# Performance work log

Measured on AMD Instinct MI355X. Metric: run time of the kernel, lower is better.

The kernel has to match this reference:

```python
import jax, jax.numpy as jnp
from jax import lax
import numpy as np

B, H, W = 8, 512, 512
COUT = 256          # backbone.out_channels
NPTS = 5 + 6        # num_vertebra_points + num_disc_points
CASC = 3            # num_cascades
PIX_MEAN, PIX_STD = 0.5, 1.0


def setup_inputs() -> dict:
    key = jax.random.key(0)
    k0, k1, k2, k3 = jax.random.split(key, 4)
    images = jax.random.normal(k0, (B, 1, H, W), jnp.float32)
    # stand-in for BackboneWithFPN level '0': stride-4 7x7 conv, 3 -> 256 ch
    backbone_w = jax.random.normal(k1, (COUT, 3, 7, 7), jnp.float32) * 0.05
    backbone_b = jnp.zeros((COUT,), jnp.float32)
    # self.fc: 1x1 conv, 256 -> 11 keypoint score channels
    fc_w = jax.random.normal(k2, (NPTS, COUT), jnp.float32) * 0.05
    fc_b = jnp.zeros((NPTS,), jnp.float32)
    # cascade heads: Linear(256, 2) per cascade
    head_w = jax.random.normal(k3, (CASC, COUT, 2), jnp.float32) * 0.02
    head_b = jnp.zeros((CASC, 2), jnp.float32)
    return dict(images=images, backbone_w=backbone_w, backbone_b=backbone_b,
                fc_w=fc_w, fc_b=fc_b, head_w=head_w, head_b=head_b)


def _resize_bilinear_ac(x, oh, ow):
    # bilinear, align_corners=True, matching F.interpolate
    b, c, h, w = x.shape
    ys = jnp.linspace(0.0, h - 1.0, oh)
    xs = jnp.linspace(0.0, w - 1.0, ow)
    y0 = jnp.floor(ys).astype(jnp.int32); y1 = jnp.minimum(y0 + 1, h - 1)
    x0 = jnp.floor(xs).astype(jnp.int32); x1 = jnp.minimum(x0 + 1, w - 1)
    wy = (ys - y0.astype(x.dtype))[:, None]          # (oh,1)
    wx = (xs - x0.astype(x.dtype))                   # (ow,)
    top = x[:, :, y0, :] * (1.0 - wy) + x[:, :, y1, :] * wy   # (b,c,oh,w)
    return top[:, :, :, x0] * (1.0 - wx) + top[:, :, :, x1] * wx


def _extract_point_feature(fm, coords, height, width):
    # fm: (B,C,fh,fw); coords: (B,P,2) with (width, height) order
    fh, fw = fm.shape[-2:]
    hi = jnp.clip(jnp.round(coords[:, :, 1] * (fh / height)).astype(jnp.int32), 0, fh - 1)
    wi = jnp.clip(jnp.round(coords[:, :, 0] * (fw / width)).astype(jnp.int32), 0, fw - 1)
    fm_t = fm.transpose(0, 2, 3, 1)                  # (B,fh,fw,C)
    return jax.vmap(lambda f, a, b: f[a, b])(fm_t, hi, wi)  # (B,P,C)


def reference(images, backbone_w, backbone_b, fc_w, fc_b, head_w, head_b):
    b = images.shape[0]
    x = (images - PIX_MEAN) / PIX_STD
    x = jnp.broadcast_to(x, (b, 3, H, W))            # .expand(-1,3,-1,-1)
    fm = lax.conv_general_dilated(
        x, backbone_w, window_strides=(4, 4), padding=((3, 3), (3, 3)),
        dimension_numbers=('NCHW', 'OIHW', 'NCHW')) + backbone_b[None, :, None, None]
    scores = jnp.einsum('bchw,kc->bkhw', fm, fc_w) + fc_b[None, :, None, None]
    scores = _resize_bilinear_ac(scores, H, W)
    heat = jax.nn.sigmoid(scores)
    # SpinalModelBase: per-channel argmax -> (width, height) coords
    idx = jnp.argmax(heat.reshape(b, NPTS, -1), axis=-1)
    coords = jnp.stack([idx % W, idx // W], axis=-1).astype(jnp.float32)  # (B,P,2)
    # cascades: gather point features, tiny Linear shift, update coords
    for i in range(CASC):
        feats = _extract_point_feature(fm, coords, H, W)     # (B,P,C)
        shift = feats @ head_w[i] + head_b[i]                # (B,P,2)
        coords = coords + shift
    return coords  # final cascade output, float (B, NPTS, 2)
```

## Files before the change

### kernel.cpp

```cpp
#include <hip/hip_runtime.h>
#include <hip/hip_bf16.h>
#include <math.h>

#define BATCH 8
#define HH 512
#define WW 512
#define COUT 256
#define NPTS 11
#define CASC 3
#define FH 128
#define FW 128
#define KT 49
#define NBK (BATCH*NPTS)
#define NSPLIT 8
#define OROWS (HH/NSPLIT)

#define FOLD_OFF   0
#define SCORES_OFF 1024
#define PVAL_OFF   (1024 + 1441792)
#define PIDX_OFF   (PVAL_OFF + 704)

#define STEPC (127.0f/511.0f)

__global__ __launch_bounds__(256) void fold_kernel(
    const float* __restrict__ bw, const float* __restrict__ bb,
    const float* __restrict__ fcw, const float* __restrict__ fcb,
    const float* __restrict__ hw, const float* __restrict__ hb,
    float* __restrict__ fold) {
  int id = blockIdx.x*4 + (threadIdx.x >> 6);
  if (id >= 850) return;
  int row = id / 50, t = id % 50;
  int lane = threadIdx.x & 63;
  float acc = 0.f;
  for (int c = lane; c < COUT; c += 64) {
    float coef;
    if (row < NPTS) {
      coef = fcw[row*COUT + c];
    } else {
      int r = row - NPTS;
      coef = hw[(r >> 1)*(COUT*2) + c*2 + (r & 1)];
    }
    float wsum;
    if (t < KT) {
      const float* p = bw + c*(3*KT) + t;
      wsum = p[0] + p[KT] + p[2*KT];
    } else {
      wsum = bb[c];
    }
    acc += coef * wsum;
  }
  #pragma unroll
  for (int off = 32; off > 0; off >>= 1) acc += __shfl_down(acc, off);
  if (lane == 0) {
    if (t == KT) acc += (row < NPTS) ? fcb[row] : hb[row - NPTS];
    if (row < NPTS) {
      if (t < KT) fold[row*KT + t] = acc;
      else        fold[NPTS*KT + row] = acc;
    } else {
      int r = row - NPTS;
      if (t < KT) fold[550 + r*KT + t] = acc;
      else        fold[844 + r] = acc;
    }
  }
}

__global__ __launch_bounds__(256) void scores_kernel(
    const float* __restrict__ img, const float* __restrict__ fold,
    float* __restrict__ scores) {
  int g = blockIdx.x*256 + threadIdx.x;
  int b = g >> 14;
  int rem = g & 16383;
  int y = rem >> 7, x = rem & 127;
  const float* im = img + (size_t)b * (HH*WW);
  float acc[NPTS];
  #pragma unroll
  for (int k = 0; k < NPTS; ++k) acc[k] = fold[NPTS*KT + k];
  int iy0 = y*4 - 3, ix0 = x*4 - 3;
  #pragma unroll
  for (int kh = 0; kh < 7; ++kh) {
    int iy = iy0 + kh;
    if (iy < 0 || iy >= HH) continue;
    #pragma unroll
    for (int kw = 0; kw < 7; ++kw) {
      int ix = ix0 + kw;
      if (ix < 0 || ix >= WW) continue;
      float xv = im[iy*WW + ix] - 0.5f;
      int t = kh*7 + kw;
      #pragma unroll
      for (int k = 0; k < NPTS; ++k) acc[k] = fmaf(fold[k*KT + t], xv, acc[k]);
    }
  }
  float* out = scores + (size_t)b * (NPTS*FH*FW) + rem;
  #pragma unroll
  for (int k = 0; k < NPTS; ++k) out[(size_t)k*(FH*FW)] = acc[k];
}

__global__ __launch_bounds__(256) void argmax_kernel(
    const float* __restrict__ scores, float* __restrict__ pval,
    int* __restrict__ pidx) {
  __shared__ __align__(16) float s[20*128];
  __shared__ float wv[4];
  __shared__ int   wi[4];
  int bk = blockIdx.x / NSPLIT;
  int q  = blockIdx.x % NSPLIT;
  const float* src = scores + (size_t)bk * (FH*FW);

  int oyb = q*OROWS;
  int ybase = (int)((float)oyb * STEPC);
  int ylast = (int)((float)(oyb + OROWS - 1) * STEPC);
  int yend  = min(ylast + 1, FH - 1);
  int rows  = yend - ybase + 1;
  {
    const float4* src4 = (const float4*)(src + ybase*FW);
    float4* s4 = (float4*)s;
    int n4 = (rows*FW) >> 2;
    for (int i = threadIdx.x; i < n4; i += 256) s4[i] = src4[i];
  }
  __syncthreads();

  int ox0 = threadIdx.x*2, ox1 = ox0 + 1;
  float tx0 = (float)ox0 * STEPC, tx1 = (float)ox1 * STEPC;
  int xa0 = (int)tx0, xb0 = (int)tx1;
  float wx0 = tx0 - (float)xa0, wx1 = tx1 - (float)xb0;
  int xa1 = min(xa0 + 1, FW - 1), xb1 = min(xb0 + 1, FW - 1);
  float omwx0 = 1.f - wx0, omwx1 = 1.f - wx1;

  float best = -3.4028235e38f;
  int bidx = 0x7fffffff;
  int prevY0 = -1;
  float a0=0.f, b0=0.f, c0=0.f, d0=0.f;
  float a1=0.f, b1=0.f, c1=0.f, d1=0.f;
  for (int j = 0; j < OROWS; ++j) {
    int oy = oyb + j;
    float ty = (float)oy * STEPC;
    int y0 = (int)ty;
    float wy = ty - (float)y0;
    float omwy = 1.f - wy;
    if (y0 != prevY0) {
      int y1 = min(y0 + 1, FH - 1);
      const float* r0 = s + (y0 - ybase)*FW;
      const float* r1 = s + (y1 - ybase)*FW;
      a0 = r0[xa0]; b0 = r1[xa0]; c0 = r0[xa1]; d0 = r1[xa1];
      a1 = r0[xb0]; b1 = r1[xb0]; c1 = r0[xb1]; d1 = r1[xb1];
      prevY0 = y0;
    }
    {
      float top0 = a0*omwy + b0*wy;
      float top1 = c0*omwy + d0*wy;
      float v = top0*omwx0 + top1*wx0;
      if (v > best) { best = v; bidx = oy*512 + ox0; }
    }
    {
      float top0 = a1*omwy + b1*wy;
      float top1 = c1*omwy + d1*wy;
      float v = top0*omwx1 + top1*wx1;
      if (v > best) { best = v; bidx = oy*512 + ox1; }
    }
  }

  #pragma unroll
  for (int off = 32; off > 0; off >>= 1) {
    float ov = __shfl_down(best, off);
    int   oi = __shfl_down(bidx, off);
    if (ov > best || (ov == best && oi < bidx)) { best = ov; bidx = oi; }
  }
  int wave = threadIdx.x >> 6;
  if ((threadIdx.x & 63) == 0) { wv[wave] = best; wi[wave] = bidx; }
  __syncthreads();
  if (threadIdx.x == 0) {
    best = wv[0]; bidx = wi[0];
    #pragma unroll
    for (int w = 1; w < 4; ++w) {
      float ov = wv[w]; int oi = wi[w];
      if (ov > best || (ov == best && oi < bidx)) { best = ov; bidx = oi; }
    }
    pval[bk*NSPLIT + q] = best;
    pidx[bk*NSPLIT + q] = bidx;
  }
}

__global__ __launch_bounds__(128) void cascade_kernel(
    const float* __restrict__ img, const float* __restrict__ fold,
    const float* __restrict__ pval, const int* __restrict__ pidx,
    float* __restrict__ out) {
  int p = threadIdx.x;
  if (p >= NBK) return;
  float best = pval[p*NSPLIT]; int bidx = pidx[p*NSPLIT];
  #pragma unroll
  for (int q = 1; q < NSPLIT; ++q) {
    float v = pval[p*NSPLIT + q]; int i = pidx[p*NSPLIT + q];
    if (v > best || (v == best && i < bidx)) { best = v; bidx = i; }
  }
  float cx = (float)(bidx & 511);
  float cy = (float)(bidx >> 9);
  int b = p / NPTS;
  const float* im = img + (size_t)b * (HH*WW);
  for (int i = 0; i < CASC; ++i) {
    float ry = rintf(cy * 0.25f), rx = rintf(cx * 0.25f);
    int hi = (int)fminf(fmaxf(ry, 0.f), (float)(FH - 1));
    int wi = (int)fminf(fmaxf(rx, 0.f), (float)(FW - 1));
    float s0 = fold[844 + i*2 + 0];
    float s1 = fold[844 + i*2 + 1];
    int iy0 = hi*4 - 3, ix0 = wi*4 - 3;
    for (int kh = 0; kh < 7; ++kh) {
      int iy = iy0 + kh;
      if (iy < 0 || iy >= HH) continue;
      for (int kw = 0; kw < 7; ++kw) {
        int ix = ix0 + kw;
        if (ix < 0 || ix >= WW) continue;
        float xv = im[iy*WW + ix] - 0.5f;
        int t = kh*7 + kw;
        s0 = fmaf(fold[550 + (i*2 + 0)*KT + t], xv, s0);
        s1 = fmaf(fold[550 + (i*2 + 1)*KT + t], xv, s1);
      }
    }
    cx += s0;
    cy += s1;
  }
  out[p*2 + 0] = cx;
  out[p*2 + 1] = cy;
}

extern "C" void kernel_launch(void* const* d_in, const int* in_sizes, int n_in,
                              void* d_out, int out_size, void* d_ws, size_t ws_size,
                              hipStream_t stream) {
  const float* img = (const float*)d_in[0];
  const float* bw  = (const float*)d_in[1];
  const float* bb  = (const float*)d_in[2];
  const float* fcw = (const float*)d_in[3];
  const float* fcb = (const float*)d_in[4];
  const float* hw  = (const float*)d_in[5];
  const float* hb  = (const float*)d_in[6];
  float* out = (float*)d_out;

  float* ws     = (float*)d_ws;
  float* fold   = ws + FOLD_OFF;
  float* scores = ws + SCORES_OFF;
  float* pval   = ws + PVAL_OFF;
  int*   pidx   = (int*)(ws + PIDX_OFF);

  fold_kernel<<<213, 256, 0, stream>>>(bw, bb, fcw, fcb, hw, hb, fold);
  scores_kernel<<<512, 256, 0, stream>>>(img, fold, scores);
  argmax_kernel<<<NBK*NSPLIT, 256, 0, stream>>>(scores, pval, pidx);
  cascade_kernel<<<1, 128, 0, stream>>>(img, fold, pval, pidx, out);
}
```

Before: 121.8 us.

## Evaluate bilinear argmax only at source-cell endpoint rows and columns

Bilinear interpolation is linear between neighbouring source samples. So the maximum over output pixels within each source cell must sit at the first or last output row and column mapped to that cell. The argmax kernel now has each thread own one endpoint column and loops over source rows, evaluating only the endpoint output rows instead of all upsampled rows and columns. The folded weights are also transposed to a tap-major layout so the per-tap coefficient reads in the scores kernel are contiguous across keypoints. The risk is tie-breaking and rounding differences against a full scan, though results should match in the exact case.

```diff
diff --git a/kernel.cpp b/kernel.cpp
--- a/kernel.cpp
+++ b/kernel.cpp
@@ -54,7 +54,7 @@
   if (lane == 0) {
     if (t == KT) acc += (row < NPTS) ? fcb[row] : hb[row - NPTS];
     if (row < NPTS) {
-      if (t < KT) fold[row*KT + t] = acc;
+      if (t < KT) fold[t*NPTS + row] = acc;
       else        fold[NPTS*KT + row] = acc;
     } else {
       int r = row - NPTS;
@@ -87,7 +87,7 @@
       float xv = im[iy*WW + ix] - 0.5f;
       int t = kh*7 + kw;
       #pragma unroll
-      for (int k = 0; k < NPTS; ++k) acc[k] = fmaf(fold[k*KT + t], xv, acc[k]);
+      for (int k = 0; k < NPTS; ++k) acc[k] = fmaf(fold[t*NPTS + k], xv, acc[k]);
     }
   }
   float* out = scores + (size_t)b * (NPTS*FH*FW) + rem;
@@ -99,8 +99,8 @@
     const float* __restrict__ scores, float* __restrict__ pval,
     int* __restrict__ pidx) {
   __shared__ __align__(16) float s[20*128];
-  __shared__ float wv[4];
-  __shared__ int   wi[4];
+  __shared__ float wvv[4];
+  __shared__ int   wvi[4];
   int bk = blockIdx.x / NSPLIT;
   int q  = blockIdx.x % NSPLIT;
   const float* src = scores + (size_t)bk * (FH*FW);
@@ -118,43 +118,45 @@
   }
   __syncthreads();
 
-  int ox0 = threadIdx.x*2, ox1 = ox0 + 1;
-  float tx0 = (float)ox0 * STEPC, tx1 = (float)ox1 * STEPC;
-  int xa0 = (int)tx0, xb0 = (int)tx1;
-  float wx0 = tx0 - (float)xa0, wx1 = tx1 - (float)xb0;
-  int xa1 = min(xa0 + 1, FW - 1), xb1 = min(xb0 + 1, FW - 1);
-  float omwx0 = 1.f - wx0, omwx1 = 1.f - wx1;
+  int t = threadIdx.x;
+  int kb = t >> 1;
+  int cf = (kb*511 + 126)/127;
+  int cl = (kb < 127) ? ((kb + 1)*511 + 126)/127 - 1 : 511;
+  int ox = (t & 1) ? cl : cf;
+  float tx = (float)ox * STEPC;
+  int xa0 = (int)tx;
+  float wx = tx - (float)xa0;
+  int xa1 = min(xa0 + 1, FW - 1);
+  float omwx = 1.f - wx;
 
   float best = -3.4028235e38f;
   int bidx = 0x7fffffff;
-  int prevY0 = -1;
-  float a0=0.f, b0=0.f, c0=0.f, d0=0.f;
-  float a1=0.f, b1=0.f, c1=0.f, d1=0.f;
-  for (int j = 0; j < OROWS; ++j) {
-    int oy = oyb + j;
-    float ty = (float)oy * STEPC;
-    int y0 = (int)ty;
-    float wy = ty - (float)y0;
-    float omwy = 1.f - wy;
-    if (y0 != prevY0) {
-      int y1 = min(y0 + 1, FH - 1);
-      const float* r0 = s + (y0 - ybase)*FW;
-      const float* r1 = s + (y1 - ybase)*FW;
-      a0 = r0[xa0]; b0 = r1[xa0]; c0 = r0[xa1]; d0 = r1[xa1];
-      a1 = r0[xb0]; b1 = r1[xb0]; c1 = r0[xb1]; d1 = r1[xb1];
-      prevY0 = y0;
-    }
-    {
-      float top0 = a0*omwy + b0*wy;
-      float top1 = c0*omwy + d0*wy;
-      float v = top0*omwx0 + top1*wx0;
-      if (v > best) { best = v; bidx = oy*512 + ox0; }
-    }
-    {
-      float top0 = a1*omwy + b1*wy;
-      float top1 = c1*omwy + d1*wy;
-      float v = top0*omwx1 + top1*wx1;
-      if (v > best) { best = v; bidx = oy*512 + ox1; }
+  for (int k = ybase; k <= ylast; ++k) {
+    int y1 = min(k + 1, FH - 1);
+    const float* r0 = s + (k  - ybase)*FW;
+    const float* r1 = s + (y1 - ybase)*FW;
+    float A = r0[xa0], B = r1[xa0], C = r0[xa1], D = r1[xa1];
+    int rf = (k*511 + 126)/127;
+    int rl = (k < 127) ? ((k + 1)*511 + 126)/127 - 1 : 511;
+    if (rf >= oyb && rf < oyb + OROWS) {
+      float ty = (float)rf * STEPC;
+      int y0i = (int)ty;
+      float wy = ty - (float)y0i;
+      float omwy = 1.f - wy;
+      float top0 = A*omwy + B*wy;
+      float top1 = C*omwy + D*wy;
+      float v = top0*omwx + top1*wx;
+      if (v > best) { best = v; bidx = rf*512 + ox; }
+    }
+    if (rl != rf && rl >= oyb && rl < oyb + OROWS) {
+      float ty = (float)rl * STEPC;
+      int y0i = (int)ty;
+      float wy = ty - (float)y0i;
+      float omwy = 1.f - wy;
+      float top0 = A*omwy + B*wy;
+      float top1 = C*omwy + D*wy;
+      float v = top0*omwx + top1*wx;
+      if (v > best) { best = v; bidx = rl*512 + ox; }
     }
   }
 
@@ -165,13 +167,13 @@
     if (ov > best || (ov == best && oi < bidx)) { best = ov; bidx = oi; }
   }
   int wave = threadIdx.x >> 6;
-  if ((threadIdx.x & 63) == 0) { wv[wave] = best; wi[wave] = bidx; }
+  if ((threadIdx.x & 63) == 0) { wvv[wave] = best; wvi[wave] = bidx; }
   __syncthreads();
   if (threadIdx.x == 0) {
-    best = wv[0]; bidx = wi[0];
+    best = wvv[0]; bidx = wvi[0];
     #pragma unroll
     for (int w = 1; w < 4; ++w) {
-      float ov = wv[w]; int oi = wi[w];
+      float ov = wvv[w]; int oi = wvi[w];
       if (ov > best || (ov == best && oi < bidx)) { best = ov; bidx = oi; }
     }
     pval[bk*NSPLIT + q] = best;
```

Result: faster. 119.2 us (-2.2%).
